# Kernel optimization log

Measured on AMD Instinct MI355X. Metric: run time of the kernel, lower is better.

## Reference

```python
import jax, jax.numpy as jnp
import numpy as np

C = 256
CQK = C // 8  # query/key channels


def setup_inputs() -> dict:
    key = jax.random.key(0)
    ks = jax.random.split(key, 7)
    B, H, W = 4, 64, 64
    x = jax.random.normal(ks[0], (B, C, H, W), dtype=jnp.float32)
    # 1x1 conv weights stored as [out_ch, in_ch] (kernel spatial dims are 1)
    sc = 1.0 / np.sqrt(C)
    Wq = jax.random.uniform(ks[1], (CQK, C), jnp.float32, -sc, sc)
    bq = jax.random.uniform(ks[2], (CQK,), jnp.float32, -sc, sc)
    Wk = jax.random.uniform(ks[3], (CQK, C), jnp.float32, -sc, sc)
    bk = jax.random.uniform(ks[4], (CQK,), jnp.float32, -sc, sc)
    Wv = jax.random.uniform(ks[5], (C, C), jnp.float32, -sc, sc)
    bv = jax.random.uniform(ks[6], (C,), jnp.float32, -sc, sc)
    gamma = jnp.zeros((1,), dtype=jnp.float32)
    return {"x": x, "Wq": Wq, "bq": bq, "Wk": Wk, "bk": bk, "Wv": Wv, "bv": bv, "gamma": gamma}


def reference(x, Wq, bq, Wk, bk, Wv, bv, gamma):
    B, Ch, H, W = x.shape
    N = H * W
    xf = x.reshape(B, Ch, N)  # [B, C, N]
    # 1x1 convs == per-pixel linear projections
    q = jnp.einsum('oc,bcn->bno', Wq, xf) + bq  # [B, N, CQK]
    k = jnp.einsum('oc,bcn->bon', Wk, xf) + bk[None, :, None]  # [B, CQK, N]
    v = jnp.einsum('oc,bcn->bon', Wv, xf) + bv[None, :, None]  # [B, C, N]
    s = jnp.einsum('bnd,bdm->bnm', q, k)  # [B, N, N]
    attn = jax.nn.softmax(s, axis=-1)
    # out[b,c,i] = sum_j v[b,c,j] * attn[b,i,j]
    out = jnp.einsum('bcj,bij->bci', v, attn).reshape(B, Ch, H, W)
    return x + gamma[0] * out
```

## Files before the change

### kernel.cpp

```cpp
#include <hip/hip_runtime.h>
#include <math.h>

#define BATCH 4
#define CCH   256
#define DQK   32
#define NPIX  4096
#define LOG2E 1.44269504088896340736f

typedef __attribute__((ext_vector_type(8)))  short          short8_t;
typedef __attribute__((ext_vector_type(4)))  unsigned short ushort4_t;
typedef __attribute__((ext_vector_type(8)))  unsigned short ushort8_t;
typedef __attribute__((ext_vector_type(16))) float          f32x16;
typedef __attribute__((ext_vector_type(2)))  unsigned int   uint2_t;

#if __has_builtin(__builtin_amdgcn_exp2f)
#define EXP2F(x) __builtin_amdgcn_exp2f(x)
#else
#define EXP2F(x) exp2f(x)
#endif

#define MFMA32(a, b, c) __builtin_amdgcn_mfma_f32_32x32x16_bf16(a, b, c, 0, 0, 0)

static __device__ __forceinline__ unsigned short f2bf(float f) {
    union { float f; unsigned int u; } v; v.f = f;
    unsigned int r = v.u + 0x7FFFu + ((v.u >> 16) & 1u);
    return (unsigned short)(r >> 16);
}

static __device__ __forceinline__ short8_t cat8(ushort4_t a, ushort4_t b) {
    ushort8_t c = __builtin_shufflevector(a, b, 0, 1, 2, 3, 4, 5, 6, 7);
    short8_t r; __builtin_memcpy(&r, &c, 16); return r;
}

static __device__ __forceinline__ short8_t u4_to_s8(const unsigned int* u) {
    short8_t r; __builtin_memcpy(&r, u, 16); return r;
}

static __device__ __forceinline__ uint2_t plswap(unsigned int a, unsigned int b) {
#if __has_builtin(__builtin_amdgcn_permlane32_swap)
    return __builtin_amdgcn_permlane32_swap(a, b, false, false);
#else
    const unsigned int sa = (unsigned int)__shfl_xor((int)a, 32);
    const unsigned int sb = (unsigned int)__shfl_xor((int)b, 32);
    const int h = (threadIdx.x >> 5) & 1;
    uint2_t r;
    r.x = h ? sb : a;
    r.y = h ? b : sa;
    return r;
#endif
}

static __device__ __forceinline__ void make_bfrag(
    const f32x16& s, float& l0, float& l1, unsigned int bfr[2][4])
{
    float pv[16];
    #pragma unroll
    for (int r = 0; r < 16; ++r) pv[r] = EXP2F(s[r]);
    #pragma unroll
    for (int r = 0; r < 16; r += 2) { l0 += pv[r]; l1 += pv[r + 1]; }
    unsigned int P[8];
    #pragma unroll
    for (int v = 0; v < 8; ++v)
        P[v] = __builtin_amdgcn_perm(__float_as_uint(pv[2 * v + 1]),
                                     __float_as_uint(pv[2 * v]), 0x07060302u);
    #pragma unroll
    for (int kp = 0; kp < 2; ++kp) {
        const uint2_t r02 = plswap(P[4 * kp + 0], P[4 * kp + 2]);
        const uint2_t r13 = plswap(P[4 * kp + 1], P[4 * kp + 3]);
        bfr[kp][0] = r02.x; bfr[kp][1] = r13.x;
        bfr[kp][2] = r02.y; bfr[kp][3] = r13.y;
    }
}

__global__ __launch_bounds__(256) void wconv_kernel(
    const float* __restrict__ Wq, const float* __restrict__ Wk,
    const float* __restrict__ Wv, unsigned short* __restrict__ wbf)
{
    const int idx = blockIdx.x * 256 + threadIdx.x;
    const int o = idx >> 8, c = idx & 255;
    float v;
    if (o < 32)      v = Wq[o * 256 + c] * LOG2E;
    else if (o < 64) v = Wk[(o - 32) * 256 + c];
    else             v = Wv[(o - 64) * 256 + c];
    wbf[((c >> 3) * 320 + o) * 8 + (c & 7)] = f2bf(v);
}

__global__ __launch_bounds__(320) void xtproj_kernel(
    const float* __restrict__ x, const unsigned short* __restrict__ wbf,
    const float* __restrict__ bq, const float* __restrict__ bk,
    const float* __restrict__ bv,
    unsigned short* __restrict__ qfrag, unsigned short* __restrict__ kfrag,
    unsigned short* __restrict__ vfrag)
{
    __shared__ unsigned short xls[2][32][32][8];
    __shared__ unsigned short qkb[2 * 2 * 32 * 40];
    __shared__ unsigned short vbuf[4 * 64 * 72];

    const int b   = blockIdx.x >> 6;
    const int nt0 = (blockIdx.x & 63) << 1;
    const int n0  = nt0 << 5;
    const int t   = threadIdx.x;
    const int w = t >> 6, lane = t & 63, il = lane & 31, h = lane >> 5;

    for (int q = t; q < 4096; q += 320) {
        const int c  = q >> 4;
        const int n4 = (q & 15) << 2;
        const float4 f = *(const float4*)&x[((size_t)(b * CCH + c)) * NPIX + n0 + n4];
        unsigned short* dst = &xls[n4 >> 5][c >> 3][n4 & 31][c & 7];
        dst[0]  = f2bf(f.x);
        dst[8]  = f2bf(f.y);
        dst[16] = f2bf(f.z);
        dst[24] = f2bf(f.w);
    }

    float4 bA[4], bB[4];
    #pragma unroll
    for (int g = 0; g < 4; ++g) {
        if (w == 0) {
            bA[g] = *(const float4*)&bq[8 * g + 4 * h];
            bB[g] = *(const float4*)&bk[8 * g + 4 * h];
        } else {
            bA[g] = *(const float4*)&bv[(w - 1) * 64 + 8 * g + 4 * h];
            bB[g] = *(const float4*)&bv[(w - 1) * 64 + 32 + 8 * g + 4 * h];
        }
    }

    f32x16 acc[2][2];
    #pragma unroll
    for (int a = 0; a < 2; ++a)
        #pragma unroll
        for (int i = 0; i < 2; ++i)
            #pragma unroll
            for (int r = 0; r < 16; ++r) acc[a][i][r] = 0.f;

    __syncthreads();

    const unsigned short* wp = wbf + ((size_t)(h * 320 + w * 64 + il)) * 8;

    #pragma unroll 4
    for (int ks = 0; ks < 16; ++ks) {
        const short8_t af0 = *(const short8_t*)(wp + ks * 5120);
        const short8_t af1 = *(const short8_t*)(wp + ks * 5120 + 256);
        const short8_t bf0 = *(const short8_t*)&xls[0][2 * ks + h][il][0];
        const short8_t bf1 = *(const short8_t*)&xls[1][2 * ks + h][il][0];
        acc[0][0] = MFMA32(af0, bf0, acc[0][0]);
        acc[0][1] = MFMA32(af0, bf1, acc[0][1]);
        acc[1][0] = MFMA32(af1, bf0, acc[1][0]);
        acc[1][1] = MFMA32(af1, bf1, acc[1][1]);
    }

    if (w == 0) {
        #pragma unroll
        for (int it = 0; it < 2; ++it)
            #pragma unroll
            for (int r = 0; r < 16; ++r) {
                const int d = (r & 3) + 8 * (r >> 2) + 4 * h;
                qkb[(it * 2 + 0) * 1280 + il * 40 + d] =
                    f2bf(acc[0][it][r] + bA[r >> 2][r & 3] * LOG2E);
                qkb[(it * 2 + 1) * 1280 + il * 40 + d] =
                    f2bf(acc[1][it][r] + bB[r >> 2][r & 3]);
            }
        #pragma unroll
        for (int it = 0; it < 2; ++it)
            #pragma unroll
            for (int rep = 0; rep < 2; ++rep) {
                const int u = rep * 64 + lane;
                const int slot = u >> 5, n = u & 31;
                ushort4_t qlo = *(const ushort4_t*)&qkb[(it * 2) * 1280 + n * 40 + slot * 8];
                ushort4_t qhi = *(const ushort4_t*)&qkb[(it * 2) * 1280 + n * 40 + slot * 8 + 4];
                ushort4_t klo = *(const ushort4_t*)&qkb[(it * 2 + 1) * 1280 + n * 40 + slot * 8];
                ushort4_t khi = *(const ushort4_t*)&qkb[(it * 2 + 1) * 1280 + n * 40 + slot * 8 + 4];
                const size_t o8 = (((size_t)(b * 128 + nt0 + it) * 4 + slot) * 32 + n) * 8;
                *(short8_t*)(qfrag + o8) = cat8(qlo, qhi);
                *(short8_t*)(kfrag + o8) = cat8(klo, khi);
            }
    } else {
        unsigned short* vb = vbuf + (w - 1) * 64 * 72;
        #pragma unroll
        for (int it = 0; it < 2; ++it)
            #pragma unroll
            for (int r = 0; r < 16; ++r) {
                const int orow = (r & 3) + 8 * (r >> 2) + 4 * h;
                vb[(orow)      * 72 + it * 32 + il] = f2bf(acc[0][it][r] + bA[r >> 2][r & 3]);
                vb[(orow + 32) * 72 + it * 32 + il] = f2bf(acc[1][it][r] + bB[r >> 2][r & 3]);
            }
        #pragma unroll
        for (int rep = 0; rep < 8; ++rep) {
            const int u = rep * 64 + lane;
            const int c = u & 63, m = u >> 6;
            const int it = m >> 2, slot = m & 3;
            ushort4_t lo = *(const ushort4_t*)&vb[c * 72 + it * 32 + slot * 8];
            ushort4_t hi = *(const ushort4_t*)&vb[c * 72 + it * 32 + slot * 8 + 4];
            const size_t o8 = (((size_t)(b * 128 + nt0 + it) * 4 + slot) * 256 +
                               (w - 1) * 64 + c) * 8;
            *(short8_t*)(vfrag + o8) = cat8(lo, hi);
        }
    }
}

struct KStage { short8_t k0, k1; };

__global__ __launch_bounds__(512, 2) void attn_kernel(
    const unsigned short* __restrict__ qfrag,
    const unsigned short* __restrict__ kfrag,
    const unsigned short* __restrict__ vfrag,
    const float* __restrict__ x,
    const float* __restrict__ gamma,
    float* __restrict__ out)
{
    __shared__ float comb[8][64][17];

    const int m8 = blockIdx.x & 7;
    const int b  = m8 >> 1;
    const int itile = ((blockIdx.x >> 3) << 1) | (m8 & 1);
    const int i0 = itile << 6;
    const int t  = threadIdx.x;
    const int w = t >> 6, lane = t & 63, il = lane & 31, h = lane >> 5;
    const int it = w & 1, ci = (w >> 1) & 1, jj = w >> 2;

    short8_t qf[2];
    #pragma unroll
    for (int ks = 0; ks < 2; ++ks)
        qf[ks] = *(const short8_t*)(qfrag +
            (((size_t)(b * 128 + itile * 2 + it) * 4 + ks * 2 + h) * 32 + il) * 8);

    const size_t kbase = (size_t)(b * 128 + jj * 64) * 1024 + h * 256 + il * 8;
    const size_t vbase = (size_t)(b * 128 + jj * 64) * 8192 + h * 2048 +
                         (ci * 128 + il) * 8;

    f32x16 zf;
    #pragma unroll
    for (int r = 0; r < 16; ++r) zf[r] = 0.f;
    f32x16 acc[4];
    #pragma unroll
    for (int c4 = 0; c4 < 4; ++c4) acc[c4] = zf;
    float ls[2] = {0.f, 0.f};

    KStage A, B;
    short8_t va[4][2], vb[4][2];

    auto loadK = [&](KStage& S, int jt) {
        const unsigned short* kp = kfrag + kbase + (size_t)jt * 1024;
        S.k0 = *(const short8_t*)kp;
        S.k1 = *(const short8_t*)(kp + 512);
    };
    auto loadV = [&](short8_t (&vv)[4][2], int jt) {
        const unsigned short* vp = vfrag + vbase + (size_t)jt * 8192;
        #pragma unroll
        for (int ct = 0; ct < 4; ++ct) {
            vv[ct][0] = *(const short8_t*)(vp + ct * 256);
            vv[ct][1] = *(const short8_t*)(vp + ct * 256 + 4096);
        }
    };

    loadK(A, 0);
    loadK(B, 1);
    f32x16 sA = MFMA32(A.k0, qf[0], zf);
    sA = MFMA32(A.k1, qf[1], sA);
    f32x16 sB = MFMA32(B.k0, qf[0], zf);
    sB = MFMA32(B.k1, qf[1], sB);
    loadK(A, 2);
    loadK(B, 3);
    loadV(va, 0);
    loadV(vb, 1);

    #pragma unroll 1
    for (int jt = 0; jt < 64; jt += 2) {
        unsigned int bfA[2][4];
        make_bfrag(sA, ls[0], ls[1], bfA);
        sA = MFMA32(A.k0, qf[0], zf);
        sA = MFMA32(A.k1, qf[1], sA);
        if (jt + 4 < 64) loadK(A, jt + 4);
        __builtin_amdgcn_s_setprio(1);
        #pragma unroll
        for (int ct = 0; ct < 4; ++ct) {
            acc[ct] = MFMA32(va[ct][0], u4_to_s8(bfA[0]), acc[ct]);
            acc[ct] = MFMA32(va[ct][1], u4_to_s8(bfA[1]), acc[ct]);
        }
        __builtin_amdgcn_s_setprio(0);
        if (jt + 2 < 64) loadV(va, jt + 2);

        unsigned int bfB[2][4];
        make_bfrag(sB, ls[0], ls[1], bfB);
        sB = MFMA32(B.k0, qf[0], zf);
        sB = MFMA32(B.k1, qf[1], sB);
        if (jt + 5 < 64) loadK(B, jt + 5);
        __builtin_amdgcn_s_setprio(1);
        #pragma unroll
        for (int ct = 0; ct < 4; ++ct) {
            acc[ct] = MFMA32(vb[ct][0], u4_to_s8(bfB[0]), acc[ct]);
            acc[ct] = MFMA32(vb[ct][1], u4_to_s8(bfB[1]), acc[ct]);
        }
        __builtin_amdgcn_s_setprio(0);
        if (jt + 3 < 64) loadV(vb, jt + 3);
    }

    float l = ls[0] + ls[1];
    l += __shfl_xor(l, 32);
    const float gam = gamma[0];
    const int pw = w ^ 4;
    float lt = 0.f;

    #pragma unroll
    for (int ct = 0; ct < 4; ++ct) {
        __syncthreads();
        #pragma unroll
        for (int r = 0; r < 16; ++r) comb[w][lane][r] = acc[ct][r];
        if (ct == 0) comb[w][lane][16] = l;
        __syncthreads();
        if (ct == 0) lt = l + comb[pw][lane][16];
        if ((ct >> 1) == jj) {
            const float sc = gam / lt;
            #pragma unroll
            for (int r = 0; r < 16; ++r) {
                const float o = acc[ct][r] + comb[pw][lane][r];
                const int c = ci * 128 + ct * 32 + (r & 3) + 8 * (r >> 2) + 4 * h;
                const size_t idx = ((size_t)(b * CCH + c)) * NPIX + i0 +
                                   it * 32 + il;
                out[idx] = x[idx] + o * sc;
            }
        }
    }
}

extern "C" void kernel_launch(void* const* d_in, const int* in_sizes, int n_in,
                              void* d_out, int out_size, void* d_ws, size_t ws_size,
                              hipStream_t stream) {
    const float* x     = (const float*)d_in[0];
    const float* Wq    = (const float*)d_in[1];
    const float* bq    = (const float*)d_in[2];
    const float* Wk    = (const float*)d_in[3];
    const float* bk    = (const float*)d_in[4];
    const float* Wv    = (const float*)d_in[5];
    const float* bv    = (const float*)d_in[6];
    const float* gamma = (const float*)d_in[7];
    float* out = (float*)d_out;

    unsigned short* ws    = (unsigned short*)d_ws;
    unsigned short* wbf   = ws;
    unsigned short* qfrag = ws + 81920;
    unsigned short* kfrag = qfrag + (size_t)524288;
    unsigned short* vfrag = kfrag + (size_t)524288;

    wconv_kernel<<<dim3(320), dim3(256), 0, stream>>>(Wq, Wk, Wv, wbf);
    xtproj_kernel<<<dim3(256), dim3(320), 0, stream>>>(
        x, wbf, bq, bk, bv, qfrag, kfrag, vfrag);
    attn_kernel<<<dim3(256), dim3(512), 0, stream>>>(
        qfrag, kfrag, vfrag, x, gamma, out);
}
```

Baseline: 146.8 us.

## Split key dimension across three wave groups per block instead of two

The attention kernel now uses 768 threads (12 waves) and splits the 128 key tiles into three uneven chunks (44/42/42) rather than two halves. The partial accumulators and softmax denominators from all three groups are combined through a larger shared buffer. The software pipeline is also simplified so QK MFMAs are issued at the top of each iteration, and the s_setprio hints are removed. This aims to raise the number of resident waves per CU to hide latency, at the cost of more register pressure under launch bounds (768,3), a less deep K prefetch, and extra reduction traffic.

Result: slower. 293.6 us (+100.0%).

```diff
diff --git a/kernel.cpp b/kernel.cpp
--- a/kernel.cpp
+++ b/kernel.cpp
@@ -200,7 +200,7 @@
 
 struct KStage { short8_t k0, k1; };
 
-__global__ __launch_bounds__(512, 2) void attn_kernel(
+__global__ __launch_bounds__(768, 3) void attn_kernel(
     const unsigned short* __restrict__ qfrag,
     const unsigned short* __restrict__ kfrag,
     const unsigned short* __restrict__ vfrag,
@@ -208,7 +208,7 @@
     const float* __restrict__ gamma,
     float* __restrict__ out)
 {
-    __shared__ float comb[8][64][17];
+    __shared__ float comb[12][64][17];
 
     const int m8 = blockIdx.x & 7;
     const int b  = m8 >> 1;
@@ -216,7 +216,10 @@
     const int i0 = itile << 6;
     const int t  = threadIdx.x;
     const int w = t >> 6, lane = t & 63, il = lane & 31, h = lane >> 5;
-    const int it = w & 1, ci = (w >> 1) & 1, jj = w >> 2;
+    const int it = w & 1, ci = (w >> 1) & 1, jq = w >> 2;
+
+    const int jbeg = (jq == 0) ? 0 : 44 + (jq - 1) * 42;
+    const int nt   = (jq == 0) ? 44 : 42;
 
     short8_t qf[2];
     #pragma unroll
@@ -224,8 +227,8 @@
         qf[ks] = *(const short8_t*)(qfrag +
             (((size_t)(b * 128 + itile * 2 + it) * 4 + ks * 2 + h) * 32 + il) * 8);
 
-    const size_t kbase = (size_t)(b * 128 + jj * 64) * 1024 + h * 256 + il * 8;
-    const size_t vbase = (size_t)(b * 128 + jj * 64) * 8192 + h * 2048 +
+    const size_t kbase = (size_t)(b * 128 + jbeg) * 1024 + h * 256 + il * 8;
+    const size_t vbase = (size_t)(b * 128 + jbeg) * 8192 + h * 2048 +
                          (ci * 128 + il) * 8;
 
     f32x16 zf;
@@ -255,50 +258,41 @@
 
     loadK(A, 0);
     loadK(B, 1);
-    f32x16 sA = MFMA32(A.k0, qf[0], zf);
-    sA = MFMA32(A.k1, qf[1], sA);
-    f32x16 sB = MFMA32(B.k0, qf[0], zf);
-    sB = MFMA32(B.k1, qf[1], sB);
-    loadK(A, 2);
-    loadK(B, 3);
     loadV(va, 0);
     loadV(vb, 1);
 
     #pragma unroll 1
-    for (int jt = 0; jt < 64; jt += 2) {
+    for (int jt = 0; jt < nt; jt += 2) {
+        f32x16 sA = MFMA32(A.k0, qf[0], zf);
+        sA = MFMA32(A.k1, qf[1], sA);
+        f32x16 sB = MFMA32(B.k0, qf[0], zf);
+        sB = MFMA32(B.k1, qf[1], sB);
+        if (jt + 2 < nt) loadK(A, jt + 2);
+        if (jt + 3 < nt) loadK(B, jt + 3);
+
         unsigned int bfA[2][4];
         make_bfrag(sA, ls[0], ls[1], bfA);
-        sA = MFMA32(A.k0, qf[0], zf);
-        sA = MFMA32(A.k1, qf[1], sA);
-        if (jt + 4 < 64) loadK(A, jt + 4);
-        __builtin_amdgcn_s_setprio(1);
         #pragma unroll
         for (int ct = 0; ct < 4; ++ct) {
             acc[ct] = MFMA32(va[ct][0], u4_to_s8(bfA[0]), acc[ct]);
             acc[ct] = MFMA32(va[ct][1], u4_to_s8(bfA[1]), acc[ct]);
         }
-        __builtin_amdgcn_s_setprio(0);
-        if (jt + 2 < 64) loadV(va, jt + 2);
-
         unsigned int bfB[2][4];
         make_bfrag(sB, ls[0], ls[1], bfB);
-        sB = MFMA32(B.k0, qf[0], zf);
-        sB = MFMA32(B.k1, qf[1], sB);
-        if (jt + 5 < 64) loadK(B, jt + 5);
-        __builtin_amdgcn_s_setprio(1);
+        if (jt + 2 < nt) loadV(va, jt + 2);
         #pragma unroll
         for (int ct = 0; ct < 4; ++ct) {
             acc[ct] = MFMA32(vb[ct][0], u4_to_s8(bfB[0]), acc[ct]);
             acc[ct] = MFMA32(vb[ct][1], u4_to_s8(bfB[1]), acc[ct]);
         }
-        __builtin_amdgcn_s_setprio(0);
-        if (jt + 3 < 64) loadV(vb, jt + 3);
+        if (jt + 3 < nt) loadV(vb, jt + 3);
     }
 
     float l = ls[0] + ls[1];
     l += __shfl_xor(l, 32);
     const float gam = gamma[0];
-    const int pw = w ^ 4;
+    const int p1 = it + 2 * ci + 4 * ((jq + 1) % 3);
+    const int p2 = it + 2 * ci + 4 * ((jq + 2) % 3);
     float lt = 0.f;
 
     #pragma unroll
@@ -308,12 +302,13 @@
         for (int r = 0; r < 16; ++r) comb[w][lane][r] = acc[ct][r];
         if (ct == 0) comb[w][lane][16] = l;
         __syncthreads();
-        if (ct == 0) lt = l + comb[pw][lane][16];
-        if ((ct >> 1) == jj) {
+        if (ct == 0)
+            lt = l + comb[p1][lane][16] + comb[p2][lane][16];
+        if (jq == (ct % 3)) {
             const float sc = gam / lt;
             #pragma unroll
             for (int r = 0; r < 16; ++r) {
-                const float o = acc[ct][r] + comb[pw][lane][r];
+                const float o = acc[ct][r] + comb[p1][lane][r] + comb[p2][lane][r];
                 const int c = ci * 128 + ct * 32 + (r & 3) + 8 * (r >> 2) + 4 * h;
                 const size_t idx = ((size_t)(b * CCH + c)) * NPIX + i0 +
                                    it * 32 + il;
@@ -345,6 +340,6 @@
     wconv_kernel<<<dim3(320), dim3(256), 0, stream>>>(Wq, Wk, Wv, wbf);
     xtproj_kernel<<<dim3(256), dim3(320), 0, stream>>>(
         x, wbf, bq, bk, bv, qfrag, kfrag, vfrag);
-    attn_kernel<<<dim3(256), dim3(512), 0, stream>>>(
+    attn_kernel<<<dim3(256), dim3(768), 0, stream>>>(
         qfrag, kfrag, vfrag, x, gamma, out);
 }
```
